# Kernel tuning notes

Hardware: AMD Instinct MI355X
Metric: run time of the kernel (lower is better)

Reference implementation:

```python
import jax, jax.numpy as jnp
import numpy as np

B, S, I, H, O = 64, 512, 512, 1024, 512


def setup_inputs() -> dict:
    key = jax.random.key(0)
    ks = jax.random.split(key, 12)
    sc = 0.05  # small init scale so gates don't fully saturate
    return {
        "x": jax.random.normal(ks[0], (B, S, I), jnp.float32),
        "Wf": jax.random.normal(ks[1], (H, H + I), jnp.float32) * sc,
        "Wi": jax.random.normal(ks[2], (H, H + I), jnp.float32) * sc,
        "Wo": jax.random.normal(ks[3], (H, H + I), jnp.float32) * sc,
        "Wc": jax.random.normal(ks[4], (H, H + I), jnp.float32) * sc,
        "bf": jnp.zeros((H,), jnp.float32),
        "bi": jnp.zeros((H,), jnp.float32),
        "bo": jnp.zeros((H,), jnp.float32),
        "bc": jnp.zeros((H,), jnp.float32),
        "W_fc": jax.random.normal(ks[5], (O, H), jnp.float32) * sc,
        "b_fc": jnp.zeros((O,), jnp.float32),
    }


def reference(x, Wf, Wi, Wo, Wc, bf, bi, bo, bc, W_fc, b_fc):
    Bb, Ss, Ii = x.shape
    Hh = Wf.shape[0]
    # Fuse the 4 gate matmuls into one GEMM (same math as 4 separate matmuls).
    W = jnp.concatenate([Wf, Wi, Wo, Wc], axis=0)        # (4H, H+I)
    b = jnp.concatenate([bf, bi, bo, bc], axis=0)        # (4H,)

    def step(carry, x_t):
        h, c = carry                                     # (B,H), (B,H)
        comb = jnp.concatenate([h, x_t], axis=1)         # (B, H+I)
        g = comb @ W.T + b                               # (B, 4H)
        f, i, o, ch = jnp.split(g, 4, axis=1)
        c = jax.nn.sigmoid(f) * c + jax.nn.sigmoid(i) * jnp.tanh(ch)
        h = jax.nn.sigmoid(o) * jnp.tanh(c)
        return (h, c), h

    h0 = jnp.zeros((Bb, Hh), x.dtype)
    c0 = jnp.zeros((Bb, Hh), x.dtype)
    (h_t, c_t), hs = jax.lax.scan(step, (h0, c0), jnp.swapaxes(x, 0, 1))
    hidden_seq = jnp.swapaxes(hs, 0, 1)                  # (B, S, H)
    output = hidden_seq @ W_fc.T + b_fc                  # (B, S, O)
    return output, (h_t, c_t)
```

## Files before the change

### kernel.cpp

```cpp
#include <hip/hip_runtime.h>
#include <hip/hip_bf16.h>

typedef __attribute__((ext_vector_type(8))) __bf16 bf16x8;
typedef __attribute__((ext_vector_type(4))) float f32x4;
typedef __attribute__((ext_vector_type(4))) unsigned uint4v;
typedef unsigned long long u64;

static constexpr int BB = 64;
static constexpr int SS = 512;
static constexpr int IN = 512;
static constexpr int HH = 1024;
static constexpr int OO = 512;
static constexpr int KK = 1536;
static constexpr int G4 = 4096;
static constexpr int NBLK = 512;
static constexpr int THR = 128;
static constexpr int COLS = 16;
static constexpr int HCPB = 4;
static constexpr int RROWS = 32;
static constexpr size_t SLAB_B = (size_t)BB * HH * 2;

__device__ __forceinline__ f32x4 mfma16(bf16x8 a, bf16x8 b, f32x4 c) {
  return __builtin_amdgcn_mfma_f32_16x16x32_bf16(a, b, c, 0, 0, 0);
}
__device__ __forceinline__ float sigm(float x) { return 1.f / (1.f + __expf(-x)); }
__device__ __forceinline__ float tanh_f(float x) { return 1.f - 2.f / (1.f + __expf(2.f * x)); }
__device__ __forceinline__ bf16x8 frag2(const char* p0) {
  u64 lo = *(const u64*)p0;
  u64 hi = *(const u64*)(p0 + 256);
  uint4v u;
  u[0] = (unsigned)lo; u[1] = (unsigned)(lo >> 32);
  u[2] = (unsigned)hi; u[3] = (unsigned)(hi >> 32);
  return __builtin_bit_cast(bf16x8, u);
}


__global__ void k_convw(const float* Wf, const float* Wi, const float* Wo, const float* Wc,
                        const float* bfv, const float* biv, const float* bov, const float* bcv,
                        __bf16* Wcomb, float* biasp) {
  int p = blockIdx.x;
  int g = (p >> 2) & 3;
  int hcol = ((p >> 4) << 2) | (p & 3);
  const float* Wg = (g == 0) ? Wf : (g == 1) ? Wi : (g == 2) ? Wo : Wc;
  const float* bg = (g == 0) ? bfv : (g == 1) ? biv : (g == 2) ? bov : bcv;
  const float* src = Wg + (size_t)hcol * KK;
  for (int k = threadIdx.x; k < KK; k += 256) Wcomb[(size_t)p * KK + k] = (__bf16)src[k];
  if (threadIdx.x == 0) biasp[p] = bg[hcol];
}

__global__ void k_convx(const float* x, __bf16* xb) {
  size_t idx = (size_t)blockIdx.x * 256 + threadIdx.x;
  int k = idx & 511;
  size_t row = idx >> 9;
  int t = (int)(row >> 6), b = (int)(row & 63);
  xb[idx] = (__bf16)x[((size_t)b * SS + t) * IN + k];
}

__global__ void k_convfc(const float* Wfc, __bf16* Wfcb) {
  size_t i = (size_t)blockIdx.x * 256 + threadIdx.x;
  Wfcb[i] = (__bf16)Wfc[i];
}

__global__ void k_zeroh0(__bf16* hsb) {
  size_t i = (size_t)blockIdx.x * 256 + threadIdx.x;
  hsb[i] = (__bf16)0.f;
}

__global__ void k_diag(float* out, float v) { out[0] = v; }

__global__ __launch_bounds__(128) void k_lstm(const __bf16* __restrict__ Wcomb,
                                              const __bf16* __restrict__ xb,
                                              const float* __restrict__ biasp,
                                              __bf16* __restrict__ hsb,
                                              float* __restrict__ tail,
                                              unsigned* __restrict__ flags) {
  const int n = blockIdx.x;
  const int R = n >> 8;
  const int m = n & 255;
  const int tid = threadIdx.x;
  const int w = tid >> 6, l = tid & 63;
  const int l16 = l & 15, lk = l >> 4;
  __shared__ __bf16 wl[48 * 512];
  __shared__ float gt[32][20];
  for (int i = tid; i < COLS * (KK / 8); i += THR) {
    int c = i / 192, kch = i % 192;
    bf16x8 v = *(const bf16x8*)(Wcomb + ((size_t)(m * COLS + c)) * KK + kch * 8);
    int chunk = kch >> 2, lkw = kch & 3;
    *(bf16x8*)(wl + ((chunk * 64 + lkw * 16 + c) << 3)) = v;
  }
  const int br = tid >> 2, rr = tid & 3;
  const int arow = R * RROWS + br;
  const float bias_f = biasp[m * COLS + 0 + rr];
  const float bias_i = biasp[m * COLS + 4 + rr];
  const float bias_o = biasp[m * COLS + 8 + rr];
  const float bias_c = biasp[m * COLS + 12 + rr];
  __syncthreads();
  const int hrow = w * 16 + l16;
  const size_t aoffX = (size_t)(R * RROWS + hrow) * IN + lk * 8;
  const __bf16* wlane = wl + ((lk * 16 + l16) << 3);
  const unsigned* recflags = flags + R * 512;
  const int startC = (n >> 3) & 15;
  const f32x4 vz = {0.f, 0.f, 0.f, 0.f};
  float cst = 0.f;
  for (int t = 0; t < SS; ++t) {
    const char* hpb = (const char*)hsb + (size_t)t * SLAB_B + (size_t)R * 65536
                      + (size_t)lk * 512 + (size_t)hrow * 8;
    const __bf16* xp = xb + (size_t)t * (BB * IN);
    f32x4 a0 = vz, a1 = vz;
#pragma unroll
    for (int kc = 0; kc < IN; kc += 64) {
      bf16x8 av0 = *(const bf16x8*)(xp + aoffX + kc);
      bf16x8 av1 = *(const bf16x8*)(xp + aoffX + kc + 32);
      bf16x8 bv0 = *(const bf16x8*)(wlane + (32 + kc / 32) * 512);
      bf16x8 bv1 = *(const bf16x8*)(wlane + (33 + kc / 32) * 512);
      a0 = mfma16(av0, bv0, a0);
      a1 = mfma16(av1, bv1, a1);
    }
    {
      const unsigned tgt = (unsigned)t;
      for (;;) {
        bool ok = true;
#pragma unroll
        for (int j = 0; j < 8; ++j) {
          unsigned f = __hip_atomic_load(&recflags[l * 8 + j], __ATOMIC_RELAXED,
                                         __HIP_MEMORY_SCOPE_AGENT);
          ok &= (f >= tgt);
        }
        if (__all((int)ok)) break;
        __builtin_amdgcn_s_sleep(1);
      }
    }
    asm volatile("" ::: "memory");
#pragma unroll
    for (int i = 0; i < 16; ++i) {
      int cc = (startC + i) & 15;
      const char* pc = hpb + (size_t)cc * 4096;
      bf16x8 av0 = frag2(pc);
      bf16x8 av1 = frag2(pc + 2048);
      bf16x8 bv0 = *(const bf16x8*)(wlane + (cc * 2) * 512);
      bf16x8 bv1 = *(const bf16x8*)(wlane + (cc * 2 + 1) * 512);
      a0 = mfma16(av0, bv0, a0);
      a1 = mfma16(av1, bv1, a1);
    }
    f32x4 s = a0 + a1;
#pragma unroll
    for (int q = 0; q < 4; ++q) gt[w * 16 + lk * 4 + q][l16] = s[q];
    asm volatile("s_waitcnt lgkmcnt(0)" ::: "memory");
    float f_ = gt[br][rr] + bias_f;
    float i_ = gt[br][4 + rr] + bias_i;
    float o_ = gt[br][8 + rr] + bias_o;
    float g_ = gt[br][12 + rr] + bias_c;
    cst = sigm(f_) * cst + sigm(i_) * tanh_f(g_);
    float hv = sigm(o_) * tanh_f(cst);
    unsigned hb = (unsigned)__builtin_bit_cast(unsigned short, (__bf16)hv);
    unsigned h1 = __shfl_down(hb, 1);
    unsigned h2 = __shfl_down(hb, 2);
    unsigned h3 = __shfl_down(hb, 3);
    if (rr == 0) {
      u64 pk = (u64)hb | ((u64)h1 << 16) | ((u64)h2 << 32) | ((u64)h3 << 48);
      u64* dst = (u64*)((char*)hsb + (size_t)(t + 1) * SLAB_B
                        + (size_t)(R * 256 + m) * 256 + (size_t)br * 8);
      __hip_atomic_store(dst, pk, __ATOMIC_RELAXED, __HIP_MEMORY_SCOPE_AGENT);
    }
    if (t == SS - 1) {
      tail[(size_t)arow * HH + m * HCPB + rr] = hv;
      tail[(size_t)BB * HH + (size_t)arow * HH + m * HCPB + rr] = cst;
    }
    asm volatile("s_waitcnt vmcnt(0)" ::: "memory");
    if (t + 1 < SS && l == 0)
      __hip_atomic_store((unsigned*)&flags[R * 512 + w * 256 + m], (unsigned)(t + 1),
                         __ATOMIC_RELAXED, __HIP_MEMORY_SCOPE_AGENT);
  }
}

__global__ __launch_bounds__(256) void k_gemm_out(const __bf16* __restrict__ hsb,
                                                  const __bf16* __restrict__ Wfcb,
                                                  const float* __restrict__ bfc,
                                                  float* __restrict__ out) {
  int w = threadIdx.x >> 6, l = threadIdx.x & 63;
  int l16 = l & 15, lk = l >> 4;
  int Mbase = blockIdx.x * 64, Nbase = blockIdx.y * 64;
  int rA = Mbase + w * 16 + l16;
  int bb = rA >> 9, tt = rA & 511;
  const char* Apb = (const char*)hsb + (size_t)(tt + 1) * SLAB_B + (size_t)(bb >> 5) * 65536
                    + (size_t)(bb & 31) * 8 + (size_t)lk * 512;
  const __bf16* Bp[4];
#pragma unroll
  for (int jt = 0; jt < 4; ++jt)
    Bp[jt] = Wfcb + ((size_t)(Nbase + jt * 16 + l16)) * HH + lk * 8;
  const f32x4 vz = {0.f, 0.f, 0.f, 0.f};
  f32x4 acc[4] = {vz, vz, vz, vz};
  for (int kc = 0; kc < HH; kc += 32) {
    bf16x8 a = frag2(Apb + (size_t)kc * 64);
#pragma unroll
    for (int jt = 0; jt < 4; ++jt) {
      bf16x8 bv = *(const bf16x8*)(Bp[jt] + kc);
      acc[jt] = mfma16(a, bv, acc[jt]);
    }
  }
#pragma unroll
  for (int jt = 0; jt < 4; ++jt) {
    int col = Nbase + jt * 16 + l16;
    float badd = bfc[col];
#pragma unroll
    for (int q = 0; q < 4; ++q) {
      int rD = Mbase + w * 16 + lk * 4 + q;
      out[(size_t)rD * OO + col] = acc[jt][q] + badd;
    }
  }
}

extern "C" void kernel_launch(void* const* d_in, const int* in_sizes, int n_in,
                              void* d_out, int out_size, void* d_ws, size_t ws_size,
                              hipStream_t stream) {
  const float* x = (const float*)d_in[0];
  const float* Wf = (const float*)d_in[1];
  const float* Wi = (const float*)d_in[2];
  const float* Wo = (const float*)d_in[3];
  const float* Wc = (const float*)d_in[4];
  const float* bfv = (const float*)d_in[5];
  const float* biv = (const float*)d_in[6];
  const float* bov = (const float*)d_in[7];
  const float* bcv = (const float*)d_in[8];
  const float* Wfc = (const float*)d_in[9];
  const float* bfc = (const float*)d_in[10];
  float* out = (float*)d_out;

  char* ws = (char*)d_ws;
  size_t off = 0;
  auto take = [&](size_t bytes) -> char* {
    off = (off + 255) & ~(size_t)255;
    char* p = ws + off;
    off += bytes;
    return p;
  };
  __bf16* Wcomb = (__bf16*)take((size_t)G4 * KK * 2);
  __bf16* Wfcb = (__bf16*)take((size_t)OO * HH * 2);
  float* biasp = (float*)take((size_t)G4 * 4);
  unsigned* flags = (unsigned*)take(1024 * 4);
  __bf16* xb = (__bf16*)take((size_t)BB * SS * IN * 2);
  __bf16* hsb = (__bf16*)take((size_t)(SS + 1) * BB * HH * 2);
  if (off > ws_size) {
    hipLaunchKernelGGL(k_diag, dim3(1), dim3(1), 0, stream, out,
                       1.0e6f + (float)(ws_size >> 20));
    return;
  }

  hipMemsetAsync(flags, 0, 1024 * 4, stream);
  hipLaunchKernelGGL(k_convw, dim3(G4), dim3(256), 0, stream,
                     Wf, Wi, Wo, Wc, bfv, biv, bov, bcv, Wcomb, biasp);
  hipLaunchKernelGGL(k_convx, dim3((BB * SS * IN) / 256), dim3(256), 0, stream, x, xb);
  hipLaunchKernelGGL(k_convfc, dim3((OO * HH) / 256), dim3(256), 0, stream, Wfc, Wfcb);
  hipLaunchKernelGGL(k_zeroh0, dim3((BB * HH) / 256), dim3(256), 0, stream, hsb);

  float* tail = out + (size_t)BB * SS * OO;
  void* args[] = {(void*)&Wcomb, (void*)&xb, (void*)&biasp, (void*)&hsb,
                  (void*)&tail, (void*)&flags};
  hipError_t cerr = hipLaunchCooperativeKernel((const void*)k_lstm, dim3(NBLK), dim3(THR),
                                               args, 0, stream);
  if (cerr != hipSuccess) {
    hipLaunchKernelGGL(k_diag, dim3(1), dim3(1), 0, stream, out,
                       1.0e5f + (float)(int)cerr);
    return;
  }

  hipLaunchKernelGGL(k_gemm_out, dim3((BB * SS) / 64, OO / 64), dim3(256), 0, stream,
                     hsb, Wfcb, bfc, out);
}
```

Before: 3.537 ms.

## Replace per-step flag barrier with NaN-sentinel polling on hidden-state data

Removes the flag array and its release store. The whole hidden-state history buffer is prefilled with a bf16 NaN sentinel, and each block polls the h fragments it needs directly, re-reading only lanes that still hold the sentinel. The recurrent loads are split into two halves so the first half can be consumed while the second is fetched, and launch bounds now request 2 blocks per CU. The cost is a fill kernel over the full hidden buffer. Correctness now depends on a real h value never equal to the sentinel pattern and on each 64-bit packed store becoming visible atomically.

```diff
diff --git a/kernel.cpp b/kernel.cpp
--- a/kernel.cpp
+++ b/kernel.cpp
@@ -18,6 +18,8 @@
 static constexpr int COLS = 16;
 static constexpr int HCPB = 4;
 static constexpr int RROWS = 32;
+static constexpr unsigned SENTH = 0x7FC0u;
+static constexpr unsigned SENT32 = 0x7FC07FC0u;
 static constexpr size_t SLAB_B = (size_t)BB * HH * 2;
 
 __device__ __forceinline__ f32x4 mfma16(bf16x8 a, bf16x8 b, f32x4 c) {
@@ -25,9 +27,11 @@
 }
 __device__ __forceinline__ float sigm(float x) { return 1.f / (1.f + __expf(-x)); }
 __device__ __forceinline__ float tanh_f(float x) { return 1.f - 2.f / (1.f + __expf(2.f * x)); }
-__device__ __forceinline__ bf16x8 frag2(const char* p0) {
-  u64 lo = *(const u64*)p0;
-  u64 hi = *(const u64*)(p0 + 256);
+__device__ __forceinline__ u64 ald64(const void* p) {
+  return __hip_atomic_load((const u64*)p, __ATOMIC_RELAXED, __HIP_MEMORY_SCOPE_AGENT);
+}
+__device__ __forceinline__ bool isS(u64 v) { return ((unsigned)v & 0xFFFFu) == SENTH; }
+__device__ __forceinline__ bf16x8 comb(u64 lo, u64 hi) {
   uint4v u;
   u[0] = (unsigned)lo; u[1] = (unsigned)(lo >> 32);
   u[2] = (unsigned)hi; u[3] = (unsigned)(hi >> 32);
@@ -61,19 +65,18 @@
   Wfcb[i] = (__bf16)Wfc[i];
 }
 
-__global__ void k_zeroh0(__bf16* hsb) {
+__global__ void k_fillh(unsigned* hsb32) {
   size_t i = (size_t)blockIdx.x * 256 + threadIdx.x;
-  hsb[i] = (__bf16)0.f;
+  hsb32[i] = (i < (size_t)(BB * HH / 2)) ? 0u : SENT32;
 }
 
 __global__ void k_diag(float* out, float v) { out[0] = v; }
 
-__global__ __launch_bounds__(128) void k_lstm(const __bf16* __restrict__ Wcomb,
-                                              const __bf16* __restrict__ xb,
-                                              const float* __restrict__ biasp,
-                                              __bf16* __restrict__ hsb,
-                                              float* __restrict__ tail,
-                                              unsigned* __restrict__ flags) {
+__global__ __launch_bounds__(128, 2) void k_lstm(const __bf16* __restrict__ Wcomb,
+                                                 const __bf16* __restrict__ xb,
+                                                 const float* __restrict__ biasp,
+                                                 __bf16* __restrict__ hsb,
+                                                 float* __restrict__ tail) {
   const int n = blockIdx.x;
   const int R = n >> 8;
   const int m = n & 255;
@@ -98,8 +101,6 @@
   const int hrow = w * 16 + l16;
   const size_t aoffX = (size_t)(R * RROWS + hrow) * IN + lk * 8;
   const __bf16* wlane = wl + ((lk * 16 + l16) << 3);
-  const unsigned* recflags = flags + R * 512;
-  const int startC = (n >> 3) & 15;
   const f32x4 vz = {0.f, 0.f, 0.f, 0.f};
   float cst = 0.f;
   for (int t = 0; t < SS; ++t) {
@@ -107,6 +108,13 @@
                       + (size_t)lk * 512 + (size_t)hrow * 8;
     const __bf16* xp = xb + (size_t)t * (BB * IN);
     f32x4 a0 = vz, a1 = vz;
+    u64 A0[8], A1[8], A2[8], A3[8];
+#pragma unroll
+    for (int i = 0; i < 8; ++i) {
+      const char* pc = hpb + (size_t)i * 4096;
+      A0[i] = ald64(pc);        A1[i] = ald64(pc + 256);
+      A2[i] = ald64(pc + 2048); A3[i] = ald64(pc + 2048 + 256);
+    }
 #pragma unroll
     for (int kc = 0; kc < IN; kc += 64) {
       bf16x8 av0 = *(const bf16x8*)(xp + aoffX + kc);
@@ -116,31 +124,61 @@
       a0 = mfma16(av0, bv0, a0);
       a1 = mfma16(av1, bv1, a1);
     }
-    {
-      const unsigned tgt = (unsigned)t;
-      for (;;) {
-        bool ok = true;
-#pragma unroll
-        for (int j = 0; j < 8; ++j) {
-          unsigned f = __hip_atomic_load(&recflags[l * 8 + j], __ATOMIC_RELAXED,
-                                         __HIP_MEMORY_SCOPE_AGENT);
-          ok &= (f >= tgt);
-        }
-        if (__all((int)ok)) break;
-        __builtin_amdgcn_s_sleep(1);
+    unsigned st = 0;
+#pragma unroll
+    for (int i = 0; i < 8; ++i) {
+      st |= (unsigned)isS(A0[i]) << (i * 4 + 0);
+      st |= (unsigned)isS(A1[i]) << (i * 4 + 1);
+      st |= (unsigned)isS(A2[i]) << (i * 4 + 2);
+      st |= (unsigned)isS(A3[i]) << (i * 4 + 3);
+    }
+    while (__builtin_expect(__any((int)(st != 0u)), 0)) {
+      unsigned ns = 0;
+#pragma unroll
+      for (int i = 0; i < 8; ++i) {
+        const char* pc = hpb + (size_t)i * 4096;
+        if (st & (1u << (i * 4 + 0))) { A0[i] = ald64(pc);            ns |= (unsigned)isS(A0[i]) << (i * 4 + 0); }
+        if (st & (1u << (i * 4 + 1))) { A1[i] = ald64(pc + 256);      ns |= (unsigned)isS(A1[i]) << (i * 4 + 1); }
+        if (st & (1u << (i * 4 + 2))) { A2[i] = ald64(pc + 2048);     ns |= (unsigned)isS(A2[i]) << (i * 4 + 2); }
+        if (st & (1u << (i * 4 + 3))) { A3[i] = ald64(pc + 2048 + 256); ns |= (unsigned)isS(A3[i]) << (i * 4 + 3); }
       }
-    }
-    asm volatile("" ::: "memory");
-#pragma unroll
-    for (int i = 0; i < 16; ++i) {
-      int cc = (startC + i) & 15;
-      const char* pc = hpb + (size_t)cc * 4096;
-      bf16x8 av0 = frag2(pc);
-      bf16x8 av1 = frag2(pc + 2048);
-      bf16x8 bv0 = *(const bf16x8*)(wlane + (cc * 2) * 512);
-      bf16x8 bv1 = *(const bf16x8*)(wlane + (cc * 2 + 1) * 512);
-      a0 = mfma16(av0, bv0, a0);
-      a1 = mfma16(av1, bv1, a1);
+      st = ns;
+    }
+#pragma unroll
+    for (int i = 0; i < 8; ++i) {
+      a0 = mfma16(comb(A0[i], A1[i]), *(const bf16x8*)(wlane + (i * 2) * 512), a0);
+      a1 = mfma16(comb(A2[i], A3[i]), *(const bf16x8*)(wlane + (i * 2 + 1) * 512), a1);
+    }
+#pragma unroll
+    for (int i = 0; i < 8; ++i) {
+      const char* pc = hpb + (size_t)(i + 8) * 4096;
+      A0[i] = ald64(pc);        A1[i] = ald64(pc + 256);
+      A2[i] = ald64(pc + 2048); A3[i] = ald64(pc + 2048 + 256);
+    }
+    st = 0;
+#pragma unroll
+    for (int i = 0; i < 8; ++i) {
+      st |= (unsigned)isS(A0[i]) << (i * 4 + 0);
+      st |= (unsigned)isS(A1[i]) << (i * 4 + 1);
+      st |= (unsigned)isS(A2[i]) << (i * 4 + 2);
+      st |= (unsigned)isS(A3[i]) << (i * 4 + 3);
+    }
+    while (__builtin_expect(__any((int)(st != 0u)), 0)) {
+      unsigned ns = 0;
+#pragma unroll
+      for (int i = 0; i < 8; ++i) {
+        const char* pc = hpb + (size_t)(i + 8) * 4096;
+        if (st & (1u << (i * 4 + 0))) { A0[i] = ald64(pc);            ns |= (unsigned)isS(A0[i]) << (i * 4 + 0); }
+        if (st & (1u << (i * 4 + 1))) { A1[i] = ald64(pc + 256);      ns |= (unsigned)isS(A1[i]) << (i * 4 + 1); }
+        if (st & (1u << (i * 4 + 2))) { A2[i] = ald64(pc + 2048);     ns |= (unsigned)isS(A2[i]) << (i * 4 + 2); }
+        if (st & (1u << (i * 4 + 3))) { A3[i] = ald64(pc + 2048 + 256); ns |= (unsigned)isS(A3[i]) << (i * 4 + 3); }
+      }
+      st = ns;
+    }
+#pragma unroll
+    for (int i = 0; i < 8; ++i) {
+      a0 = mfma16(comb(A0[i], A1[i]), *(const bf16x8*)(wlane + ((i + 8) * 2) * 512), a0);
+      a1 = mfma16(comb(A2[i], A3[i]), *(const bf16x8*)(wlane + ((i + 8) * 2 + 1) * 512), a1);
     }
     f32x4 s = a0 + a1;
 #pragma unroll
@@ -166,10 +204,6 @@
       tail[(size_t)arow * HH + m * HCPB + rr] = hv;
       tail[(size_t)BB * HH + (size_t)arow * HH + m * HCPB + rr] = cst;
     }
-    asm volatile("s_waitcnt vmcnt(0)" ::: "memory");
-    if (t + 1 < SS && l == 0)
-      __hip_atomic_store((unsigned*)&flags[R * 512 + w * 256 + m], (unsigned)(t + 1),
-                         __ATOMIC_RELAXED, __HIP_MEMORY_SCOPE_AGENT);
   }
 }
 
@@ -191,7 +225,10 @@
   const f32x4 vz = {0.f, 0.f, 0.f, 0.f};
   f32x4 acc[4] = {vz, vz, vz, vz};
   for (int kc = 0; kc < HH; kc += 32) {
-    bf16x8 a = frag2(Apb + (size_t)kc * 64);
+    const char* p0 = Apb + (size_t)kc * 64;
+    u64 lo = *(const u64*)p0;
+    u64 hi = *(const u64*)(p0 + 256);
+    bf16x8 a = comb(lo, hi);
 #pragma unroll
     for (int jt = 0; jt < 4; ++jt) {
       bf16x8 bv = *(const bf16x8*)(Bp[jt] + kc);
@@ -237,7 +274,6 @@
   __bf16* Wcomb = (__bf16*)take((size_t)G4 * KK * 2);
   __bf16* Wfcb = (__bf16*)take((size_t)OO * HH * 2);
   float* biasp = (float*)take((size_t)G4 * 4);
-  unsigned* flags = (unsigned*)take(1024 * 4);
   __bf16* xb = (__bf16*)take((size_t)BB * SS * IN * 2);
   __bf16* hsb = (__bf16*)take((size_t)(SS + 1) * BB * HH * 2);
   if (off > ws_size) {
@@ -246,16 +282,15 @@
     return;
   }
 
-  hipMemsetAsync(flags, 0, 1024 * 4, stream);
   hipLaunchKernelGGL(k_convw, dim3(G4), dim3(256), 0, stream,
                      Wf, Wi, Wo, Wc, bfv, biv, bov, bcv, Wcomb, biasp);
   hipLaunchKernelGGL(k_convx, dim3((BB * SS * IN) / 256), dim3(256), 0, stream, x, xb);
   hipLaunchKernelGGL(k_convfc, dim3((OO * HH) / 256), dim3(256), 0, stream, Wfc, Wfcb);
-  hipLaunchKernelGGL(k_zeroh0, dim3((BB * HH) / 256), dim3(256), 0, stream, hsb);
+  hipLaunchKernelGGL(k_fillh, dim3(((SS + 1) * BB * HH / 2) / 256), dim3(256), 0, stream,
+                     (unsigned*)hsb);
 
   float* tail = out + (size_t)BB * SS * OO;
-  void* args[] = {(void*)&Wcomb, (void*)&xb, (void*)&biasp, (void*)&hsb,
-                  (void*)&tail, (void*)&flags};
+  void* args[] = {(void*)&Wcomb, (void*)&xb, (void*)&biasp, (void*)&hsb, (void*)&tail};
   hipError_t cerr = hipLaunchCooperativeKernel((const void*)k_lstm, dim3(NBLK), dim3(THR),
                                                args, 0, stream);
   if (cerr != hipSuccess) {
```

Measured after the change: 5.732 ms. 62.1% more time.
